# Kernel tuning notes

Hardware: AMD Instinct MI355X
Metric: run time of the kernel (lower is better)

Reference implementation:

```python
import jax, jax.numpy as jnp
import numpy as np

DIM, R, HEAD = 512, 4, 8
HD = DIM // HEAD
SCALE = HD ** -0.5
EPS = 1e-5


def dwconv(x, w, b, stride, padding):
    # depthwise conv (groups == channels) + bias + relu; x:[B,C,H,W], w:[C,1,kh,kw]
    y = jax.lax.conv_general_dilated(
        x, w, window_strides=stride, padding=padding,
        feature_group_count=x.shape[1],
        dimension_numbers=('NCHW', 'OIHW', 'NCHW'))
    return jax.nn.relu(y + b[None, :, None, None])


def setup_inputs() -> dict:
    key = jax.random.key(0)
    ks = jax.random.split(key, 12)
    s = 0.02
    return {
        'x': jax.random.normal(ks[0], (8, DIM, 56, 56), dtype=jnp.float32),
        'Wq': jax.random.normal(ks[1], (DIM, DIM), dtype=jnp.float32) * s,
        'bq': jnp.zeros((DIM,), jnp.float32),
        'Wkv': jax.random.normal(ks[2], (2 * DIM, DIM), dtype=jnp.float32) * s,
        'bkv': jnp.zeros((2 * DIM,), jnp.float32),
        'w1a': jax.random.normal(ks[3], (DIM, 1, 1, R), dtype=jnp.float32) * s,
        'b1a': jnp.zeros((DIM,), jnp.float32),
        'w1b': jax.random.normal(ks[4], (DIM, 1, R, 1), dtype=jnp.float32) * s,
        'b1b': jnp.zeros((DIM,), jnp.float32),
        'w2': jax.random.normal(ks[5], (DIM, 1, R, R), dtype=jnp.float32) * s,
        'b2': jnp.zeros((DIM,), jnp.float32),
        'w3': jax.random.normal(ks[6], (DIM, 1, 3, 3), dtype=jnp.float32) * s,
        'b3': jnp.zeros((DIM,), jnp.float32),
        'gamma': jnp.ones((DIM,), jnp.float32),
        'beta': jnp.zeros((DIM,), jnp.float32),
    }


def reference(x, Wq, bq, Wkv, bkv, w1a, b1a, w1b, b1b, w2, b2, w3, b3, gamma, beta):
    B, C, H, W = x.shape
    N = H * W
    x_layer = x.reshape(B, C, N).transpose(0, 2, 1)  # [B,N,C]
    q = (x_layer @ Wq.T + bq).reshape(B, N, HEAD, HD).transpose(0, 2, 1, 3)  # [B,h,N,d]

    # branch 1: (1,R)s(1,R) dwconv -> (R,1)s(R,1) dwconv
    l1 = dwconv(dwconv(x, w1a, b1a, (1, R), ((0, 0), (0, 0))),
                w1b, b1b, (R, 1), ((0, 0), (0, 0))).reshape(B, C, -1)
    # branch 2: RxR stride-R dwconv
    l2 = dwconv(x, w2, b2, (R, R), ((0, 0), (0, 0))).reshape(B, C, -1)
    # branch 3: avg-pool to (H/R, W/R) then 3x3 dwconv pad 1
    l3 = x.reshape(B, C, H // R, R, W // R, R).mean(axis=(3, 5))
    l3 = dwconv(l3, w3, b3, (1, 1), ((1, 1), (1, 1))).reshape(B, C, -1)

    l_ = jnp.concatenate([l1, l2, l3], axis=2).transpose(0, 2, 1)  # [B,M,C]
    mu = l_.mean(-1, keepdims=True)
    var = ((l_ - mu) ** 2).mean(-1, keepdims=True)
    l_ = (l_ - mu) * jax.lax.rsqrt(var + EPS) * gamma + beta

    M = l_.shape[1]
    kv = (l_ @ Wkv.T + bkv).reshape(B, M, 2, HEAD, HD).transpose(2, 0, 3, 1, 4)
    k, v = kv[0], kv[1]  # [B,h,M,d]

    attn = jax.nn.softmax(jnp.einsum('bhid,bhjd->bhij', q, k) * SCALE, axis=-1)
    out = jnp.einsum('bhij,bhjd->bhid', attn, v).transpose(0, 2, 1, 3).reshape(B, N, C)
    # NOTE: original torch code computes proj(out) but then overwrites it with
    # proj_drop(out); with drop=0 the returned value is exactly `out`.
    return out
```

## Files before the change

### kernel.cpp

```cpp
#include <hip/hip_runtime.h>
#include <hip/hip_bf16.h>

#define BATCH   8
#define C_DIM   512
#define HWD     56
#define NPIX    3136
#define PW      14
#define PP      196
#define M_TOT   588
#define BM_ROWS 4704
#define BM_PAD  4736
#define HEADS   8
#define HD      64
#define N_SEQ   3136
#define SM_SCALE 0.125f

#define KS_STRIDE 68
#define KS_ROWS   592
#define VS_STRIDE 596
#define ATTN_LDS_SHORTS (KS_ROWS * KS_STRIDE + 64 * VS_STRIDE)
#define ATTN_LDS_BYTES  (ATTN_LDS_SHORTS * 2)

typedef __attribute__((ext_vector_type(8))) short bf16x8;
typedef __attribute__((ext_vector_type(4))) short bf16x4;
typedef __attribute__((ext_vector_type(4))) float f32x4;

__device__ __forceinline__ short f2bs(float f) {
    __hip_bfloat16 h = __float2bfloat16(f);
    return *reinterpret_cast<short*>(&h);
}
__device__ __forceinline__ unsigned pkbf(float lo, float hi) {
    __hip_bfloat162 t = __float22bfloat162_rn(make_float2(lo, hi));
    return *reinterpret_cast<unsigned*>(&t);
}

__device__ __forceinline__ f32x4 mfma16(bf16x4 a, bf16x4 b, f32x4 c) {
#if __has_builtin(__builtin_amdgcn_mfma_f32_16x16x16bf16_1k)
    return __builtin_amdgcn_mfma_f32_16x16x16bf16_1k(a, b, c, 0, 0, 0);
#elif __has_builtin(__builtin_amdgcn_mfma_f32_16x16x16_bf16)
    return __builtin_amdgcn_mfma_f32_16x16x16_bf16(a, b, c, 0, 0, 0);
#else
    asm volatile("v_mfma_f32_16x16x16_bf16 %0, %1, %2, %0\n\ts_nop 7\n\ts_nop 1"
                 : "+v"(c) : "v"(a), "v"(b));
    return c;
#endif
}

__device__ __forceinline__ void gl_lds16(const void* g, void* l) {
    __builtin_amdgcn_global_load_lds(
        (const __attribute__((address_space(1))) void*)g,
        (__attribute__((address_space(3))) void*)l, 16, 0, 0);
}

__global__ __launch_bounds__(256) void k_branches(
    const float* __restrict__ x,
    const float* __restrict__ w1a, const float* __restrict__ b1a,
    const float* __restrict__ w1b, const float* __restrict__ b1b,
    const float* __restrict__ w2,  const float* __restrict__ b2,
    const float* __restrict__ w3,  const float* __restrict__ b3,
    float* __restrict__ l_pre)
{
    __shared__ float xs[NPIX];
    __shared__ float y1s[HWD * PW];
    __shared__ float pools[PP];
    const int c = blockIdx.x, b = blockIdx.y, tid = threadIdx.x;
    const float* xp = x + ((size_t)(b * C_DIM + c)) * NPIX;
    for (int i = tid; i < NPIX / 4; i += 256)
        ((float4*)xs)[i] = ((const float4*)xp)[i];
    __syncthreads();

    const float wa0 = w1a[c*4+0], wa1 = w1a[c*4+1], wa2 = w1a[c*4+2], wa3 = w1a[c*4+3];
    const float ba = b1a[c];
    for (int i = tid; i < HWD * PW; i += 256) {
        int h = i / PW, w = i % PW;
        const float* r = xs + h * HWD + w * 4;
        float v = ba + r[0]*wa0 + r[1]*wa1 + r[2]*wa2 + r[3]*wa3;
        y1s[i] = fmaxf(v, 0.f);
    }
    if (tid < PP) {
        int h = tid / PW, w = tid % PW;
        float s = 0.f;
        #pragma unroll
        for (int r = 0; r < 4; ++r) {
            const float* rr = xs + (h*4 + r) * HWD + w * 4;
            s += rr[0] + rr[1] + rr[2] + rr[3];
        }
        pools[tid] = s * (1.f / 16.f);
    }
    __syncthreads();

    if (tid < PP) {
        int h = tid / PW, w = tid % PW;
        float* lp = l_pre + ((size_t)(b * C_DIM + c)) * M_TOT;
        float v1 = b1b[c];
        v1 += y1s[(h*4+0)*PW + w] * w1b[c*4+0];
        v1 += y1s[(h*4+1)*PW + w] * w1b[c*4+1];
        v1 += y1s[(h*4+2)*PW + w] * w1b[c*4+2];
        v1 += y1s[(h*4+3)*PW + w] * w1b[c*4+3];
        lp[tid] = fmaxf(v1, 0.f);
        float v2 = b2[c];
        #pragma unroll
        for (int r = 0; r < 4; ++r)
            #pragma unroll
            for (int s2 = 0; s2 < 4; ++s2)
                v2 += xs[(h*4+r)*HWD + w*4 + s2] * w2[c*16 + r*4 + s2];
        lp[PP + tid] = fmaxf(v2, 0.f);
        float v3 = b3[c];
        #pragma unroll
        for (int dh = -1; dh <= 1; ++dh)
            #pragma unroll
            for (int dw = -1; dw <= 1; ++dw) {
                int hh = h + dh, ww = w + dw;
                if (hh >= 0 && hh < PW && ww >= 0 && ww < PW)
                    v3 += pools[hh*PW + ww] * w3[c*9 + (dh+1)*3 + (dw+1)];
            }
        lp[2*PP + tid] = fmaxf(v3, 0.f);
    }
}

__global__ __launch_bounds__(256) void k_stats(
    const float* __restrict__ l_pre, float2* __restrict__ stats)
{
    __shared__ float ssum[4][64];
    __shared__ float ssq[4][64];
    const int tid = threadIdx.x;
    const int ml = tid & 63, cg = tid >> 6;
    const int b = blockIdx.y;
    const int m = blockIdx.x * 64 + ml;
    float s = 0.f, q = 0.f;
    if (m < M_TOT) {
        const float* base = l_pre + ((size_t)b * C_DIM + cg * 128) * M_TOT + m;
        for (int c = 0; c < 128; ++c) {
            float v = base[(size_t)c * M_TOT];
            s += v; q += v * v;
        }
    }
    ssum[cg][ml] = s; ssq[cg][ml] = q;
    __syncthreads();
    if (tid < 64 && blockIdx.x * 64 + tid < M_TOT) {
        float ts = ssum[0][tid] + ssum[1][tid] + ssum[2][tid] + ssum[3][tid];
        float tq = ssq[0][tid] + ssq[1][tid] + ssq[2][tid] + ssq[3][tid];
        float mu = ts * (1.f / 512.f);
        float var = tq * (1.f / 512.f) - mu * mu;
        stats[(size_t)b * M_TOT + blockIdx.x * 64 + tid] =
            make_float2(mu, rsqrtf(var + 1e-5f));
    }
}

__global__ __launch_bounds__(256) void k_wconv(
    const float* __restrict__ Wq, const float* __restrict__ Wkv,
    short* __restrict__ Wqb, short* __restrict__ Wkvb)
{
    int i = (blockIdx.x * 256 + threadIdx.x) * 4;
    if (i < 262144) {
        float4 v = *(const float4*)(Wq + i);
        short o[4] = {f2bs(v.x), f2bs(v.y), f2bs(v.z), f2bs(v.w)};
        *(short4*)(Wqb + i) = *(short4*)o;
    } else {
        int j = i - 262144;
        float4 v = *(const float4*)(Wkv + j);
        short o[4] = {f2bs(v.x), f2bs(v.y), f2bs(v.z), f2bs(v.w)};
        *(short4*)(Wkvb + j) = *(short4*)o;
    }
}

__global__ __launch_bounds__(256) void k_xpose(
    const float* __restrict__ x, short* __restrict__ Xb)
{
    __shared__ float sx[64][68];
    const int tid = threadIdx.x;
    const int n0 = blockIdx.x * 64, c0 = blockIdx.y * 64, b = blockIdx.z;
    #pragma unroll
    for (int it = 0; it < 4; ++it) {
        int idx = tid + it * 256;
        int cr = idx >> 4, n4 = (idx & 15) * 4;
        float4 v = *(const float4*)(x + ((size_t)(b * C_DIM + c0 + cr)) * NPIX + n0 + n4);
        *(float4*)&sx[cr][n4] = v;
    }
    __syncthreads();
    #pragma unroll
    for (int p = 0; p < 2; ++p) {
        int idx = tid + p * 256;
        int nr = idx >> 3, cg = (idx & 7) * 8;
        short ov[8];
        #pragma unroll
        for (int e = 0; e < 8; ++e) ov[e] = f2bs(sx[cg + e][nr]);
        *(float4*)&Xb[((size_t)(b * NPIX + n0 + nr)) * C_DIM + c0 + cg] = *(float4*)ov;
    }
}

__global__ __launch_bounds__(256) void k_lnt(
    const float* __restrict__ l_pre, const float2* __restrict__ stats,
    const float* __restrict__ gamma, const float* __restrict__ beta,
    short* __restrict__ Lb)
{
    __shared__ float sx[64][68];
    const int tid = threadIdx.x;
    const int m0 = blockIdx.x * 64, c0 = blockIdx.y * 64, b = blockIdx.z;
    #pragma unroll
    for (int it = 0; it < 4; ++it) {
        int idx = tid + it * 256;
        int cr = idx >> 4, m4 = (idx & 15) * 4;
        float4 v = {0.f, 0.f, 0.f, 0.f};
        if (m0 + m4 < M_TOT)
            v = *(const float4*)(l_pre + ((size_t)(b * C_DIM + c0 + cr)) * M_TOT + m0 + m4);
        *(float4*)&sx[cr][m4] = v;
    }
    __syncthreads();
    #pragma unroll
    for (int p = 0; p < 2; ++p) {
        int idx = tid + p * 256;
        int mr = idx >> 3, cg = (idx & 7) * 8;
        int m = m0 + mr;
        float mu = 0.f, rstd = 0.f;
        if (m < M_TOT) {
            float2 st = stats[(size_t)b * M_TOT + m];
            mu = st.x; rstd = st.y;
        }
        short ov[8];
        #pragma unroll
        for (int e = 0; e < 8; ++e) {
            int c = c0 + cg + e;
            ov[e] = f2bs((sx[cg + e][mr] - mu) * rstd * gamma[c] + beta[c]);
        }
        if (m < M_TOT)
            *(float4*)&Lb[((size_t)(b * M_TOT + m)) * C_DIM + c0 + cg] = *(float4*)ov;
    }
}

__global__ __launch_bounds__(256) void k_gemm_q(
    const short* __restrict__ A, const short* __restrict__ Bw,
    const float* __restrict__ bias, short* __restrict__ Qb)
{
    __shared__ short As[128 * 64];
    __shared__ short Bs[128 * 64];
    const int tid = threadIdx.x;
    const int lane = tid & 63, w = tid >> 6;
    const int l15 = lane & 15, quad = lane >> 4;
    const int wr = w & 1, wc = w >> 1;
    const int row0 = blockIdx.x * 128, col0 = blockIdx.y * 128;
    const int lr8 = lane >> 3, lc8 = (lane & 7) * 8;

    f32x4 acc[4][4] = {};

    for (int c0 = 0; c0 < 512; c0 += 64) {
        __syncthreads();
        #pragma unroll
        for (int it = 0; it < 4; ++it) {
            int r = w * 32 + it * 8;
            gl_lds16(A  + (size_t)(row0 + r + lr8) * 512 + c0 + lc8, &As[r * 64]);
            gl_lds16(Bw + (size_t)(col0 + r + lr8) * 512 + c0 + lc8, &Bs[r * 64]);
        }
        __syncthreads();
        #pragma unroll
        for (int ks = 0; ks < 2; ++ks) {
            bf16x8 af[4], bf[4];
            #pragma unroll
            for (int t = 0; t < 4; ++t) {
                af[t] = *(const bf16x8*)&As[(wr*64 + t*16 + l15)*64 + ks*32 + quad*8];
                bf[t] = *(const bf16x8*)&Bs[(wc*64 + t*16 + l15)*64 + ks*32 + quad*8];
            }
            #pragma unroll
            for (int nt = 0; nt < 4; ++nt)
                #pragma unroll
                for (int mt = 0; mt < 4; ++mt)
                    acc[nt][mt] = __builtin_amdgcn_mfma_f32_16x16x32_bf16(
                        af[nt], bf[mt], acc[nt][mt], 0, 0, 0);
        }
    }

    #pragma unroll
    for (int nt = 0; nt < 4; ++nt) {
        int row_t = row0 + wr * 64 + nt * 16 + quad * 4;
        #pragma unroll
        for (int mt = 0; mt < 4; ++mt) {
            int col = col0 + wc * 64 + mt * 16 + l15;
            float bv = bias[col];
            int h = col >> 6, d = col & 63;
            #pragma unroll
            for (int r = 0; r < 4; ++r) {
                int row_g = row_t + r;
                int b = row_g / N_SEQ;
                int n = row_g - b * N_SEQ;
                Qb[(((size_t)(b * HEADS + h)) * N_SEQ + n) * HD + d] =
                    f2bs(acc[nt][mt][r] + bv);
            }
        }
    }
}

__global__ __launch_bounds__(256) void k_gemm_kv(
    const short* __restrict__ A, const short* __restrict__ Bw,
    const float* __restrict__ bias,
    short* __restrict__ Kb, short* __restrict__ Vt)
{
    __shared__ short As[128 * 64];
    __shared__ short Bs[128 * 64];
    const int tid = threadIdx.x;
    const int lane = tid & 63, w = tid >> 6;
    const int l15 = lane & 15, quad = lane >> 4;
    const int wr = w & 1, wc = w >> 1;
    const int row0 = blockIdx.x * 128, col0 = blockIdx.y * 128;
    const int lr8 = lane >> 3, lc8 = (lane & 7) * 8;

    f32x4 acc[4][4] = {};

    for (int c0 = 0; c0 < 512; c0 += 64) {
        __syncthreads();
        #pragma unroll
        for (int it = 0; it < 4; ++it) {
            int r = w * 32 + it * 8;
            gl_lds16(A  + (size_t)(row0 + r + lr8) * 512 + c0 + lc8, &As[r * 64]);
            gl_lds16(Bw + (size_t)(col0 + r + lr8) * 512 + c0 + lc8, &Bs[r * 64]);
        }
        __syncthreads();
        #pragma unroll
        for (int ks = 0; ks < 2; ++ks) {
            bf16x8 af[4], bf[4];
            #pragma unroll
            for (int t = 0; t < 4; ++t) {
                af[t] = *(const bf16x8*)&As[(wr*64 + t*16 + l15)*64 + ks*32 + quad*8];
                bf[t] = *(const bf16x8*)&Bs[(wc*64 + t*16 + l15)*64 + ks*32 + quad*8];
            }
            #pragma unroll
            for (int nt = 0; nt < 4; ++nt)
                #pragma unroll
                for (int mt = 0; mt < 4; ++mt)
                    acc[nt][mt] = __builtin_amdgcn_mfma_f32_16x16x32_bf16(
                        af[nt], bf[mt], acc[nt][mt], 0, 0, 0);
        }
    }

    #pragma unroll
    for (int nt = 0; nt < 4; ++nt) {
        int row_t = row0 + wr * 64 + nt * 16 + quad * 4;
        #pragma unroll
        for (int mt = 0; mt < 4; ++mt) {
            int col = col0 + wc * 64 + mt * 16 + l15;
            float bv = bias[col];
            #pragma unroll
            for (int r = 0; r < 4; ++r) {
                int row_g = row_t + r;
                float v = acc[nt][mt][r] + bv;
                if (row_g < BM_ROWS) {
                    int b = row_g / M_TOT;
                    int m = row_g - b * M_TOT;
                    if (col < 512) {
                        int h = col >> 6, d = col & 63;
                        Kb[(((size_t)(b * HEADS + h)) * M_TOT + m) * HD + d] = f2bs(v);
                    } else {
                        int jj = col - 512, h = jj >> 6, d = jj & 63;
                        Vt[(((size_t)(b * HEADS + h)) * HD + d) * M_TOT + m] = f2bs(v);
                    }
                }
            }
        }
    }
}

__global__ __launch_bounds__(1024) void k_attn(
    const short* __restrict__ Qb, const short* __restrict__ Kb,
    const short* __restrict__ Vt, float* __restrict__ out)
{
    extern __shared__ short smem[];
    short* Ks = smem;
    short* Vs = smem + KS_ROWS * KS_STRIDE;

    const int tid = threadIdx.x;
    const int lane = tid & 63, w = tid >> 6;
    const int l15 = lane & 15, quad = lane >> 4;
    const int q4 = blockIdx.x, h = blockIdx.y, b = blockIdx.z;
    const size_t bh = (size_t)(b * HEADS + h);
    const size_t kbase = bh * M_TOT * HD;
    const size_t vbase = bh * (size_t)HD * M_TOT;

    for (int i = tid; i < 4704; i += 1024) {
        int row = i >> 3, seg = i & 7;
        *(float4*)&Ks[row * KS_STRIDE + seg * 8] =
            *(const float4*)(Kb + kbase + (size_t)row * 64 + seg * 8);
    }
    if (tid < 256) {
        int r = tid >> 6, cc = tid & 63;
        Ks[(588 + r) * KS_STRIDE + cc] = 0;
    }
    {
        int row = tid >> 4, tg = tid & 15;
        const short* src = Vt + vbase + (size_t)row * M_TOT;
        #pragma unroll 2
        for (int jj = tg; jj < 147; jj += 16)
            *(float2*)&Vs[row * VS_STRIDE + jj * 4] = *(const float2*)(src + jj * 4);
    }
    if (tid < 512) {
        int row = tid >> 3, cc = tid & 7;
        Vs[row * VS_STRIDE + 588 + cc] = 0;
    }
    __syncthreads();

    for (int ds = w; ds < 25; ds += 16) {
        const bool sbv = (ds < 24);
        const int nA = q4 * 784 + ds * 32 + l15;
        const int nB = sbv ? nA + 16 : nA;

        bf16x8 qfA[2], qfB[2];
        #pragma unroll
        for (int ks = 0; ks < 2; ++ks) {
            qfA[ks] = *(const bf16x8*)(Qb + (bh * N_SEQ + nA) * HD + ks * 32 + quad * 8);
            qfB[ks] = *(const bf16x8*)(Qb + (bh * N_SEQ + nB) * HD + ks * 32 + quad * 8);
        }

        f32x4 oaccA[4] = {}, oaccB[4] = {};
        float rsA = 0.f, rsB = 0.f;

        for (int j0 = 0; j0 < KS_ROWS; j0 += 16) {
            const short* krow = &Ks[(j0 + l15) * KS_STRIDE];
            bf16x8 kf0 = *(const bf16x8*)&krow[quad * 8];
            bf16x8 kf1 = *(const bf16x8*)&krow[32 + quad * 8];

            f32x4 sA = {}, sB = {};
            sA = __builtin_amdgcn_mfma_f32_16x16x32_bf16(kf0, qfA[0], sA, 0, 0, 0);
            sB = __builtin_amdgcn_mfma_f32_16x16x32_bf16(kf0, qfB[0], sB, 0, 0, 0);
            sA = __builtin_amdgcn_mfma_f32_16x16x32_bf16(kf1, qfA[1], sA, 0, 0, 0);
            sB = __builtin_amdgcn_mfma_f32_16x16x32_bf16(kf1, qfB[1], sB, 0, 0, 0);

            const float msk = (j0 == 576 && quad == 3) ? 0.f : 1.f;
            float pA[4], pB[4];
            #pragma unroll
            for (int r = 0; r < 4; ++r) {
                pA[r] = __expf(sA[r] * SM_SCALE);
                pB[r] = __expf(sB[r] * SM_SCALE);
            }
            rsA += (pA[0] + pA[1] + pA[2] + pA[3]) * msk;
            rsB += (pB[0] + pB[1] + pB[2] + pB[3]) * msk;

            unsigned ua[2] = {pkbf(pA[0], pA[1]), pkbf(pA[2], pA[3])};
            unsigned ub[2] = {pkbf(pB[0], pB[1]), pkbf(pB[2], pB[3])};
            bf16x4 pbA, pbB;
            __builtin_memcpy(&pbA, ua, 8);
            __builtin_memcpy(&pbB, ub, 8);

            #pragma unroll
            for (int dt = 0; dt < 4; ++dt) {
                bf16x4 vf = *(const bf16x4*)&Vs[(dt * 16 + l15) * VS_STRIDE + j0 + quad * 4];
                oaccA[dt] = mfma16(vf, pbA, oaccA[dt]);
                oaccB[dt] = mfma16(vf, pbB, oaccB[dt]);
            }
        }

        rsA += __shfl_xor(rsA, 16); rsA += __shfl_xor(rsA, 32);
        rsB += __shfl_xor(rsB, 16); rsB += __shfl_xor(rsB, 32);
        const float invA = 1.f / rsA;
        const float invB = 1.f / rsB;
        float* orowA = out + ((size_t)b * N_SEQ + nA) * C_DIM + h * HD;
        #pragma unroll
        for (int dt = 0; dt < 4; ++dt) {
            float4 o;
            o.x = oaccA[dt][0] * invA; o.y = oaccA[dt][1] * invA;
            o.z = oaccA[dt][2] * invA; o.w = oaccA[dt][3] * invA;
            *(float4*)&orowA[dt * 16 + quad * 4] = o;
        }
        if (sbv) {
            float* orowB = out + ((size_t)b * N_SEQ + nB) * C_DIM + h * HD;
            #pragma unroll
            for (int dt = 0; dt < 4; ++dt) {
                float4 o;
                o.x = oaccB[dt][0] * invB; o.y = oaccB[dt][1] * invB;
                o.z = oaccB[dt][2] * invB; o.w = oaccB[dt][3] * invB;
                *(float4*)&orowB[dt * 16 + quad * 4] = o;
            }
        }
    }
}

extern "C" void kernel_launch(void* const* d_in, const int* in_sizes, int n_in,
                              void* d_out, int out_size, void* d_ws, size_t ws_size,
                              hipStream_t stream) {
    const float* x     = (const float*)d_in[0];
    const float* Wq    = (const float*)d_in[1];
    const float* bq    = (const float*)d_in[2];
    const float* Wkv   = (const float*)d_in[3];
    const float* bkv   = (const float*)d_in[4];
    const float* w1a   = (const float*)d_in[5];
    const float* b1a   = (const float*)d_in[6];
    const float* w1b   = (const float*)d_in[7];
    const float* b1b   = (const float*)d_in[8];
    const float* w2    = (const float*)d_in[9];
    const float* b2    = (const float*)d_in[10];
    const float* w3    = (const float*)d_in[11];
    const float* b3    = (const float*)d_in[12];
    const float* gamma = (const float*)d_in[13];
    const float* beta  = (const float*)d_in[14];
    float* out = (float*)d_out;

    char* ws = (char*)d_ws;
    short*  Xb    = (short*)ws;
    float*  l_pre = (float*)ws;
    float2* stats = (float2*)(ws + 9633792);
    short*  Lb    = (short*)(ws + 9671424);
    short*  Wqb   = (short*)(ws + 25690112);
    short*  Wkvb  = (short*)(ws + 26214400);
    short*  Kb    = (short*)(ws + 27262976);
    short*  Vt    = (short*)(ws + 32079872);
    short*  Qb    = (short*)(ws + 36896768);

    static bool attr_set = false;
    hipFuncSetAttribute((const void*)k_attn,
                        hipFuncAttributeMaxDynamicSharedMemorySize,
                        ATTN_LDS_BYTES);
    (void)attr_set;

    k_wconv<<<768, 256, 0, stream>>>(Wq, Wkv, Wqb, Wkvb);
    k_xpose<<<dim3(49, 8, BATCH), 256, 0, stream>>>(x, Xb);
    k_gemm_q<<<dim3(196, 4), 256, 0, stream>>>(Xb, Wqb, bq, Qb);
    k_branches<<<dim3(C_DIM, BATCH), 256, 0, stream>>>(
        x, w1a, b1a, w1b, b1b, w2, b2, w3, b3, l_pre);
    k_stats<<<dim3(10, BATCH), 256, 0, stream>>>(l_pre, stats);
    k_lnt<<<dim3(10, 8, BATCH), 256, 0, stream>>>(l_pre, stats, gamma, beta, Lb);
    k_gemm_kv<<<dim3(37, 8), 256, 0, stream>>>(Lb, Wkvb, bkv, Kb, Vt);
    k_attn<<<dim3(4, HEADS, BATCH), 1024, ATTN_LDS_BYTES, stream>>>(Qb, Kb, Vt, out);
}
```

Before: 275.1 us.

## Fold softmax scale into Q, use exp2, MFMA row-sum, software-pipeline LDS loads

Folds the softmax scale and log2(e) into the Q projection epilogue so the attention loop can use a raw exp2 without any multiply. Row sums are computed with an extra MFMA against a vector of ones instead of scalar adds and cross-lane shuffles, with the padded key rows' contribution subtracted afterwards. The K/V LDS loads are double-buffered across two 16-key steps so they overlap the MFMA work. This trades extra MFMA issue slots and registers for fewer VALU ops and less load latency, and the padding correction relies on the padded keys producing exp2(0)=1.

```diff
diff --git a/kernel.cpp b/kernel.cpp
--- a/kernel.cpp
+++ b/kernel.cpp
@@ -14,6 +14,7 @@
 #define HD      64
 #define N_SEQ   3136
 #define SM_SCALE 0.125f
+#define SM_SCALE_LOG2E 0.1803368801111204f
 
 #define KS_STRIDE 68
 #define KS_ROWS   592
@@ -32,6 +33,13 @@
 __device__ __forceinline__ unsigned pkbf(float lo, float hi) {
     __hip_bfloat162 t = __float22bfloat162_rn(make_float2(lo, hi));
     return *reinterpret_cast<unsigned*>(&t);
+}
+__device__ __forceinline__ float fexp2(float x) {
+#if __has_builtin(__builtin_amdgcn_exp2f)
+    return __builtin_amdgcn_exp2f(x);
+#else
+    return exp2f(x);
+#endif
 }
 
 __device__ __forceinline__ f32x4 mfma16(bf16x4 a, bf16x4 b, f32x4 c) {
@@ -283,7 +291,7 @@
                 int b = row_g / N_SEQ;
                 int n = row_g - b * N_SEQ;
                 Qb[(((size_t)(b * HEADS + h)) * N_SEQ + n) * HD + d] =
-                    f2bs(acc[nt][mt][r] + bv);
+                    f2bs((acc[nt][mt][r] + bv) * SM_SCALE_LOG2E);
             }
         }
     }
@@ -396,6 +404,8 @@
     }
     __syncthreads();
 
+    const bf16x4 ones = {(short)0x3F80, (short)0x3F80, (short)0x3F80, (short)0x3F80};
+
     for (int ds = w; ds < 25; ds += 16) {
         const bool sbv = (ds < 24);
         const int nA = q4 * 784 + ds * 32 + l15;
@@ -409,47 +419,69 @@
         }
 
         f32x4 oaccA[4] = {}, oaccB[4] = {};
-        float rsA = 0.f, rsB = 0.f;
-
-        for (int j0 = 0; j0 < KS_ROWS; j0 += 16) {
-            const short* krow = &Ks[(j0 + l15) * KS_STRIDE];
-            bf16x8 kf0 = *(const bf16x8*)&krow[quad * 8];
-            bf16x8 kf1 = *(const bf16x8*)&krow[32 + quad * 8];
-
+        f32x4 rsaccA = {}, rsaccB = {};
+
+        auto LOAD = [&](int j0, bf16x8& K0, bf16x8& K1,
+                        bf16x4& V0, bf16x4& V1, bf16x4& V2, bf16x4& V3) {
+            const short* kr = &Ks[(j0 + l15) * KS_STRIDE + quad * 8];
+            K0 = *(const bf16x8*)kr;
+            K1 = *(const bf16x8*)(kr + 32);
+            const short* vr = &Vs[l15 * VS_STRIDE + j0 + quad * 4];
+            V0 = *(const bf16x4*)vr;
+            V1 = *(const bf16x4*)(vr + 16 * VS_STRIDE);
+            V2 = *(const bf16x4*)(vr + 32 * VS_STRIDE);
+            V3 = *(const bf16x4*)(vr + 48 * VS_STRIDE);
+        };
+
+        auto STEP = [&](bf16x8 K0, bf16x8 K1,
+                        bf16x4 V0, bf16x4 V1, bf16x4 V2, bf16x4 V3) {
             f32x4 sA = {}, sB = {};
-            sA = __builtin_amdgcn_mfma_f32_16x16x32_bf16(kf0, qfA[0], sA, 0, 0, 0);
-            sB = __builtin_amdgcn_mfma_f32_16x16x32_bf16(kf0, qfB[0], sB, 0, 0, 0);
-            sA = __builtin_amdgcn_mfma_f32_16x16x32_bf16(kf1, qfA[1], sA, 0, 0, 0);
-            sB = __builtin_amdgcn_mfma_f32_16x16x32_bf16(kf1, qfB[1], sB, 0, 0, 0);
-
-            const float msk = (j0 == 576 && quad == 3) ? 0.f : 1.f;
+            sA = __builtin_amdgcn_mfma_f32_16x16x32_bf16(K0, qfA[0], sA, 0, 0, 0);
+            sB = __builtin_amdgcn_mfma_f32_16x16x32_bf16(K0, qfB[0], sB, 0, 0, 0);
+            sA = __builtin_amdgcn_mfma_f32_16x16x32_bf16(K1, qfA[1], sA, 0, 0, 0);
+            sB = __builtin_amdgcn_mfma_f32_16x16x32_bf16(K1, qfB[1], sB, 0, 0, 0);
+
             float pA[4], pB[4];
             #pragma unroll
             for (int r = 0; r < 4; ++r) {
-                pA[r] = __expf(sA[r] * SM_SCALE);
-                pB[r] = __expf(sB[r] * SM_SCALE);
-            }
-            rsA += (pA[0] + pA[1] + pA[2] + pA[3]) * msk;
-            rsB += (pB[0] + pB[1] + pB[2] + pB[3]) * msk;
-
+                pA[r] = fexp2(sA[r]);
+                pB[r] = fexp2(sB[r]);
+            }
             unsigned ua[2] = {pkbf(pA[0], pA[1]), pkbf(pA[2], pA[3])};
             unsigned ub[2] = {pkbf(pB[0], pB[1]), pkbf(pB[2], pB[3])};
             bf16x4 pbA, pbB;
             __builtin_memcpy(&pbA, ua, 8);
             __builtin_memcpy(&pbB, ub, 8);
 
-            #pragma unroll
-            for (int dt = 0; dt < 4; ++dt) {
-                bf16x4 vf = *(const bf16x4*)&Vs[(dt * 16 + l15) * VS_STRIDE + j0 + quad * 4];
-                oaccA[dt] = mfma16(vf, pbA, oaccA[dt]);
-                oaccB[dt] = mfma16(vf, pbB, oaccB[dt]);
-            }
-        }
-
-        rsA += __shfl_xor(rsA, 16); rsA += __shfl_xor(rsA, 32);
-        rsB += __shfl_xor(rsB, 16); rsB += __shfl_xor(rsB, 32);
-        const float invA = 1.f / rsA;
-        const float invB = 1.f / rsB;
+            rsaccA = mfma16(ones, pbA, rsaccA);
+            rsaccB = mfma16(ones, pbB, rsaccB);
+
+            oaccA[0] = mfma16(V0, pbA, oaccA[0]);
+            oaccB[0] = mfma16(V0, pbB, oaccB[0]);
+            oaccA[1] = mfma16(V1, pbA, oaccA[1]);
+            oaccB[1] = mfma16(V1, pbB, oaccB[1]);
+            oaccA[2] = mfma16(V2, pbA, oaccA[2]);
+            oaccB[2] = mfma16(V2, pbB, oaccB[2]);
+            oaccA[3] = mfma16(V3, pbA, oaccA[3]);
+            oaccB[3] = mfma16(V3, pbB, oaccB[3]);
+        };
+
+        bf16x8 k0a, k1a, k0b, k1b;
+        bf16x4 v0a, v1a, v2a, v3a, v0b, v1b, v2b, v3b;
+
+        LOAD(0, k0a, k1a, v0a, v1a, v2a, v3a);
+        #pragma unroll 1
+        for (int t = 0; t < 18; ++t) {
+            const int j0 = t * 32;
+            LOAD(j0 + 16, k0b, k1b, v0b, v1b, v2b, v3b);
+            STEP(k0a, k1a, v0a, v1a, v2a, v3a);
+            LOAD(j0 + 32, k0a, k1a, v0a, v1a, v2a, v3a);
+            STEP(k0b, k1b, v0b, v1b, v2b, v3b);
+        }
+        STEP(k0a, k1a, v0a, v1a, v2a, v3a);
+
+        const float invA = 1.f / (rsaccA[0] - 4.f);
+        const float invB = 1.f / (rsaccB[0] - 4.f);
         float* orowA = out + ((size_t)b * N_SEQ + nA) * C_DIM + h * HD;
         #pragma unroll
         for (int dt = 0; dt < 4; ++dt) {
```

Result: faster. 269.1 us (-2.2%).
